# Kernel tuning notes

Measured on AMD Instinct MI355X. Metric: run time of the kernel, lower is better.

Reference implementation:

```python
import jax, jax.numpy as jnp
import numpy as np

EPS = 1e-15

def gmm_conv(x, row, col, pseudo, g_w, mu, sigma, root_w, bias):
    # x: [N,Fin], pseudo: [E,D], g_w: [Fin,K*Fout], mu/sigma: [K,D], root_w: [Fin,Fout]
    N = x.shape[0]
    K, D = mu.shape
    Fout = g_w.shape[1] // K
    gx = (x @ g_w).reshape(N, K, Fout)                       # per-node kernel transforms
    diff = pseudo[:, None, :] - mu[None, :, :]               # [E,K,D]
    gauss = jnp.exp(-0.5 * jnp.sum(diff * diff / (EPS + sigma[None] ** 2), axis=-1))  # [E,K]
    msg = jnp.einsum('ek,eko->eo', gauss, gx[row])           # [E,Fout]
    agg = jax.ops.segment_sum(msg, col, num_segments=N)      # scatter-add to targets
    cnt = jax.ops.segment_sum(jnp.ones((msg.shape[0],), x.dtype), col, num_segments=N)
    agg = agg / jnp.maximum(cnt, 1.0)[:, None]               # mean aggregation (GMMConv default)
    return agg + x @ root_w + bias

def setup_inputs() -> dict:
    key = jax.random.key(0)
    ks = jax.random.split(key, 12)
    N, E, F, H, C, K, D = 50000, 800000, 128, 64, 16, 8, 2
    return {
        'x': jax.random.normal(ks[0], (N, F), jnp.float32),
        'edge_index': jax.random.randint(ks[1], (2, E), 0, N, jnp.int64),
        'edge_attr': jax.random.uniform(ks[2], (E, D), jnp.float32),
        'g1_w': jax.random.normal(ks[3], (F, K * H), jnp.float32) * 0.1,
        'mu1': jax.random.normal(ks[4], (K, D), jnp.float32),
        'sigma1': jax.random.uniform(ks[5], (K, D), jnp.float32) + 0.5,
        'root1_w': jax.random.normal(ks[6], (F, H), jnp.float32) * 0.1,
        'bias1': jnp.zeros((H,), jnp.float32),
        'g2_w': jax.random.normal(ks[7], (H, K * C), jnp.float32) * 0.1,
        'mu2': jax.random.normal(ks[8], (K, D), jnp.float32),
        'sigma2': jax.random.uniform(ks[9], (K, D), jnp.float32) + 0.5,
        'root2_w': jax.random.normal(ks[10], (H, C), jnp.float32) * 0.1,
        'bias2': jnp.zeros((C,), jnp.float32),
    }

def reference(x, edge_index, edge_attr, g1_w, mu1, sigma1, root1_w, bias1,
              g2_w, mu2, sigma2, root2_w, bias2):
    row, col = edge_index[0], edge_index[1]
    # dropout p applied in eval mode -> identity
    h = jax.nn.elu(gmm_conv(x, row, col, edge_attr, g1_w, mu1, sigma1, root1_w, bias1))
    out = gmm_conv(h, row, col, edge_attr, g2_w, mu2, sigma2, root2_w, bias2)
    return jax.nn.log_softmax(out, axis=1)
```

## Files before the change

### kernel.cpp

```cpp
#include <hip/hip_runtime.h>
#include <hip/hip_bf16.h>
#include <hip/hip_fp16.h>
#include <math.h>


#define NF 128
#define NH 64
#define NC 16
#define Z1NODES 16
#define Z1CAP 448
#define E2NODES 16
#define E2CAP 320
#define GXST 160

typedef __bf16 v8bf __attribute__((ext_vector_type(8)));
typedef float v4f __attribute__((ext_vector_type(4)));

__device__ inline ushort f2bu(float x) {
  __hip_bfloat16 h = __float2bfloat16(x);
  return *(ushort*)&h;
}
__device__ inline uint packh2(float a, float b) {
  __half ha = __float2half_rn(a), hb = __float2half_rn(b);
  return (uint)(*(ushort*)&ha) | ((uint)(*(ushort*)&hb) << 16);
}
__device__ inline float2 unph2(uint u) {
  ushort a = (ushort)(u & 0xffff), b = (ushort)(u >> 16);
  return make_float2(__half2float(*(__half*)&a), __half2float(*(__half*)&b));
}
__device__ inline v8bf ld_frag(const ushort* p) {
  uint4 u = *(const uint4*)p;
  return __builtin_bit_cast(v8bf, u);
}

__global__ __launch_bounds__(256) void hist_kernel(const int* __restrict__ col,
                                                   int* __restrict__ counts, int E) {
  int e = blockIdx.x * 256 + threadIdx.x;
  if (e < E) atomicAdd(&counts[col[e]], 1);
}

__global__ __launch_bounds__(256) void scan1_kernel(const int* __restrict__ counts,
                                                    int* __restrict__ starts,
                                                    int* __restrict__ bsums) {
  __shared__ int wsum[4];
  const int t = threadIdx.x, lane = t & 63, wv = t >> 6;
  int4 v = ((const int4*)counts)[blockIdx.x * 256 + t];
  int tsum = v.x + v.y + v.z + v.w;
  int inc = tsum;
  #pragma unroll
  for (int off = 1; off < 64; off <<= 1) {
    int u = __shfl_up(inc, off, 64);
    if (lane >= off) inc += u;
  }
  if (lane == 63) wsum[wv] = inc;
  __syncthreads();
  int wpre = 0;
  for (int j = 0; j < wv; ++j) wpre += wsum[j];
  int excl = wpre + inc - tsum;
  int4 o;
  o.x = excl; o.y = o.x + v.x; o.z = o.y + v.y; o.w = o.z + v.z;
  ((int4*)starts)[blockIdx.x * 256 + t] = o;
  if (t == 255) bsums[blockIdx.x] = excl + tsum;
}

__global__ __launch_bounds__(64) void scan2_kernel(const int* __restrict__ bsums,
                                                   int* __restrict__ bofs, int NB) {
  int lane = threadIdx.x;
  int v = (lane < NB) ? bsums[lane] : 0;
  int inc = v;
  #pragma unroll
  for (int off = 1; off < 64; off <<= 1) {
    int u = __shfl_up(inc, off, 64);
    if (lane >= off) inc += u;
  }
  if (lane < NB) bofs[lane] = inc - v;
}

__global__ __launch_bounds__(256) void scan3_kernel(int* __restrict__ starts,
                                                    int* __restrict__ cursor,
                                                    const int* __restrict__ bofs) {
  int add = bofs[blockIdx.x];
  int idx = blockIdx.x * 256 + threadIdx.x;
  int4 s = ((int4*)starts)[idx];
  s.x += add; s.y += add; s.z += add; s.w += add;
  ((int4*)starts)[idx] = s;
  ((int4*)cursor)[idx] = s;
}

__global__ __launch_bounds__(256) void fill_kernel(
    const int* __restrict__ row, const int* __restrict__ col,
    const float* __restrict__ eattr,
    const float* __restrict__ mu1, const float* __restrict__ sg1,
    const float* __restrict__ mu2, const float* __restrict__ sg2,
    int* __restrict__ cursor, int* __restrict__ erow,
    uint4* __restrict__ ew1, uint4* __restrict__ ew2, int E) {
  int e = blockIdx.x * 256 + threadIdx.x;
  if (e >= E) return;
  int c = col[e];
  int pos = atomicAdd(&cursor[c], 1);
  float p0 = eattr[2 * e], p1 = eattr[2 * e + 1];
  float w1[8], w2[8];
  #pragma unroll
  for (int k = 0; k < 8; ++k) {
    float d0 = p0 - mu1[2 * k], d1 = p1 - mu1[2 * k + 1];
    float s0 = sg1[2 * k], s1 = sg1[2 * k + 1];
    w1[k] = __expf(-0.5f * (d0 * d0 / (1e-15f + s0 * s0) +
                            d1 * d1 / (1e-15f + s1 * s1)));
    float e0 = p0 - mu2[2 * k], e1 = p1 - mu2[2 * k + 1];
    float t0 = sg2[2 * k], t1 = sg2[2 * k + 1];
    w2[k] = __expf(-0.5f * (e0 * e0 / (1e-15f + t0 * t0) +
                            e1 * e1 / (1e-15f + t1 * t1)));
  }
  erow[pos] = row[e];
  ew1[pos] = make_uint4(packh2(w1[0], w1[1]), packh2(w1[2], w1[3]),
                        packh2(w1[4], w1[5]), packh2(w1[6], w1[7]));
  ew2[pos] = make_uint4(packh2(w2[0], w2[1]), packh2(w2[2], w2[3]),
                        packh2(w2[4], w2[5]), packh2(w2[6], w2[7]));
}

__global__ __launch_bounds__(256) void cast_x_kernel(const float* __restrict__ x,
                                                     ushort* __restrict__ A1, int N) {
  int idx = blockIdx.x * 256 + threadIdx.x;
  if (idx >= N * 32) return;
  int n = idx >> 5, c4 = idx & 31;
  float4 v = ((const float4*)x)[idx];
  ushort4 o;
  o.x = f2bu(v.x); o.y = f2bu(v.y); o.z = f2bu(v.z); o.w = f2bu(v.w);
  *(ushort4*)(A1 + (size_t)n * 1152 + 1024 + c4 * 4) = o;
}

__global__ __launch_bounds__(256) void prep_kernel(
    const float* __restrict__ g1w, const float* __restrict__ r1w,
    const float* __restrict__ g2w, const float* __restrict__ r2w,
    ushort* __restrict__ W1t, ushort* __restrict__ G2pT) {
  int i = blockIdx.x * 256 + threadIdx.x;
  if (i < 64 * 1152) {
    int h = i / 1152, j = i % 1152;
    float v = (j < 1024) ? g1w[(size_t)(j & 127) * 512 + (j >> 7) * 64 + h]
                         : r1w[(size_t)(j - 1024) * 64 + h];
    W1t[i] = f2bu(v);
  } else {
    int i2 = i - 64 * 1152;
    if (i2 < 144 * 64) {
      int cp = i2 / 64, f = i2 % 64;
      float v;
      if (cp < 128) {
        int kq = cp >> 5, rem = cp & 31;
        int o = rem >> 1, k = kq * 2 + (rem & 1);
        v = g2w[(size_t)f * 128 + k * 16 + o];
      } else {
        v = r2w[(size_t)f * 16 + (cp - 128)];
      }
      G2pT[i2] = f2bu(v);
    }
  }
}

__global__ __launch_bounds__(256) void z1_kernel(
    ushort* __restrict__ A1, const int* __restrict__ erow,
    const uint4* __restrict__ ew1, const int* __restrict__ starts, int N) {
  __shared__ __align__(16) float lw[Z1CAP + 8][8];
  __shared__ int loff[Z1CAP + 8];
  const int t = threadIdx.x, lane = t & 63, wv = t >> 6;
  const int base = (int)blockIdx.x * Z1NODES;
  const int S = starts[base];
  const int cl = min(starts[base + Z1NODES] - S, Z1CAP);
  for (int i = t; i < cl; i += 256) {
    loff[i] = erow[S + i] * 2304;
    uint4 qq = ew1[S + i];
    float2 a = unph2(qq.x), b = unph2(qq.y), c = unph2(qq.z), d = unph2(qq.w);
    *(float4*)&lw[i][0] = make_float4(a.x, a.y, b.x, b.y);
    *(float4*)&lw[i][4] = make_float4(c.x, c.y, d.x, d.y);
  }
  if (t < 8) {
    loff[cl + t] = 0;
    *(float4*)&lw[cl + t][0] = make_float4(0.f, 0.f, 0.f, 0.f);
    *(float4*)&lw[cl + t][4] = make_float4(0.f, 0.f, 0.f, 0.f);
  }
  __syncthreads();

  const char* xb = (const char*)(A1 + 1024) + (lane << 2);

  for (int i = 0; i < Z1NODES / 4; ++i) {
    const int n = base + wv * 4 + i;
    const int be = starts[n], ee = starts[n + 1];
    float a0[8], a1[8];
    #pragma unroll
    for (int k = 0; k < 8; ++k) { a0[k] = 0.f; a1[k] = 0.f; }

    const int reRel = min(ee - S, cl);
    for (int q = min(be - S, cl); q < reRel; q += 8) {
      int off[8];
      #pragma unroll
      for (int u = 0; u < 8; ++u) off[u] = loff[q + u];
      uint g[8];
      #pragma unroll
      for (int u = 0; u < 8; ++u) g[u] = *(const uint*)(xb + off[u]);
      #pragma unroll
      for (int u = 0; u < 8; ++u) {
        const bool ok = (q + u) < reRel;
        float4 wl = *(float4*)&lw[q + u][0];
        float4 wh = *(float4*)&lw[q + u][4];
        float f0 = ok ? __uint_as_float(g[u] << 16) : 0.f;
        float f1 = ok ? __uint_as_float(g[u] & 0xffff0000u) : 0.f;
        a0[0] = fmaf(wl.x, f0, a0[0]); a1[0] = fmaf(wl.x, f1, a1[0]);
        a0[1] = fmaf(wl.y, f0, a0[1]); a1[1] = fmaf(wl.y, f1, a1[1]);
        a0[2] = fmaf(wl.z, f0, a0[2]); a1[2] = fmaf(wl.z, f1, a1[2]);
        a0[3] = fmaf(wl.w, f0, a0[3]); a1[3] = fmaf(wl.w, f1, a1[3]);
        a0[4] = fmaf(wh.x, f0, a0[4]); a1[4] = fmaf(wh.x, f1, a1[4]);
        a0[5] = fmaf(wh.y, f0, a0[5]); a1[5] = fmaf(wh.y, f1, a1[5]);
        a0[6] = fmaf(wh.z, f0, a0[6]); a1[6] = fmaf(wh.z, f1, a1[6]);
        a0[7] = fmaf(wh.w, f0, a0[7]); a1[7] = fmaf(wh.w, f1, a1[7]);
      }
    }
    for (int j = max(S + reRel, be); j < ee; ++j) {
      uint4 qq = ew1[j];
      uint g = *(const uint*)(xb + erow[j] * 2304);
      float2 a = unph2(qq.x), b = unph2(qq.y), c = unph2(qq.z), d = unph2(qq.w);
      float f0 = __uint_as_float(g << 16);
      float f1 = __uint_as_float(g & 0xffff0000u);
      a0[0] = fmaf(a.x, f0, a0[0]); a1[0] = fmaf(a.x, f1, a1[0]);
      a0[1] = fmaf(a.y, f0, a0[1]); a1[1] = fmaf(a.y, f1, a1[1]);
      a0[2] = fmaf(b.x, f0, a0[2]); a1[2] = fmaf(b.x, f1, a1[2]);
      a0[3] = fmaf(b.y, f0, a0[3]); a1[3] = fmaf(b.y, f1, a1[3]);
      a0[4] = fmaf(c.x, f0, a0[4]); a1[4] = fmaf(c.x, f1, a1[4]);
      a0[5] = fmaf(c.y, f0, a0[5]); a1[5] = fmaf(c.y, f1, a1[5]);
      a0[6] = fmaf(d.x, f0, a0[6]); a1[6] = fmaf(d.x, f1, a1[6]);
      a0[7] = fmaf(d.y, f0, a0[7]); a1[7] = fmaf(d.y, f1, a1[7]);
    }
    const float inv = 1.f / fmaxf((float)(ee - be), 1.f);
    ushort* zr = A1 + (size_t)n * 1152;
    #pragma unroll
    for (int k = 0; k < 8; ++k) {
      uint pk = (uint)f2bu(a0[k] * inv) | ((uint)f2bu(a1[k] * inv) << 16);
      *(uint*)(zr + k * 128 + 2 * lane) = pk;
    }
  }
}

__global__ __launch_bounds__(256) void gemm1_mfma(
    const ushort* __restrict__ A1, const ushort* __restrict__ W1t,
    const float* __restrict__ b1, ushort* __restrict__ h_bf, int N) {
  __shared__ __align__(16) ushort As[2][64 * 32];
  __shared__ __align__(16) ushort Bs[2][64 * 32];
  const int t = threadIdx.x, lane = t & 63, wv = t >> 6;
  const int mfrag = lane & 15, quad = lane >> 4;
  const int m0 = (int)blockIdx.x * 64;
  const int st_r = t >> 2, st_c = (t & 3) * 8;
  const int st_o = st_r * 32 + st_c;
  const ushort* ag = A1 + (size_t)(m0 + st_r) * 1152 + st_c;
  const ushort* bg = W1t + (size_t)st_r * 1152 + st_c;

  {
    uint4 a0 = *(const uint4*)ag;
    uint4 b0 = *(const uint4*)bg;
    *(uint4*)(&As[0][st_o]) = a0;
    *(uint4*)(&Bs[0][st_o]) = b0;
  }
  __syncthreads();

  v4f acc[4];
  #pragma unroll
  for (int ct = 0; ct < 4; ++ct) acc[ct] = (v4f){0.f, 0.f, 0.f, 0.f};

  for (int kc = 0; kc < 36; ++kc) {
    const int cb = kc & 1, nb = cb ^ 1;
    uint4 an, bn;
    if (kc < 35) {
      an = *(const uint4*)(ag + (kc + 1) * 32);
      bn = *(const uint4*)(bg + (kc + 1) * 32);
    }
    v8bf a = ld_frag(&As[cb][(wv * 16 + mfrag) * 32 + quad * 8]);
    #pragma unroll
    for (int ct = 0; ct < 4; ++ct) {
      v8bf b = ld_frag(&Bs[cb][(ct * 16 + mfrag) * 32 + quad * 8]);
      acc[ct] = __builtin_amdgcn_mfma_f32_16x16x32_bf16(a, b, acc[ct], 0, 0, 0);
    }
    if (kc < 35) {
      *(uint4*)(&As[nb][st_o]) = an;
      *(uint4*)(&Bs[nb][st_o]) = bn;
      __syncthreads();
    }
  }
  #pragma unroll
  for (int ct = 0; ct < 4; ++ct) {
    const int colh = ct * 16 + mfrag;
    const float bc = b1[colh];
    #pragma unroll
    for (int r = 0; r < 4; ++r) {
      int node = m0 + wv * 16 + quad * 4 + r;
      if (node < N) {
        float v = acc[ct][r] + bc;
        v = v > 0.f ? v : expm1f(v);
        h_bf[(size_t)node * NH + colh] = f2bu(v);
      }
    }
  }
}

__global__ __launch_bounds__(256) void gemm2a_kernel(
    const ushort* __restrict__ h_bf, const ushort* __restrict__ G2pT,
    ushort* __restrict__ gx2e, int N) {
  const int t = threadIdx.x, lane = t & 63, wv = t >> 6;
  const int mfrag = lane & 15, quad = lane >> 4;
  const int m0 = (int)blockIdx.x * 64 + wv * 16;
  v4f acc[9];
  #pragma unroll
  for (int t9 = 0; t9 < 9; ++t9) acc[t9] = (v4f){0.f, 0.f, 0.f, 0.f};
  const ushort* arow = h_bf + (size_t)(m0 + mfrag) * 64 + quad * 8;
  const ushort* brow = G2pT + (size_t)mfrag * 64 + quad * 8;
  #pragma unroll
  for (int kc = 0; kc < 2; ++kc) {
    v8bf a = ld_frag(arow + kc * 32);
    #pragma unroll
    for (int t9 = 0; t9 < 9; ++t9) {
      v8bf b = ld_frag(brow + (size_t)t9 * 16 * 64 + kc * 32);
      acc[t9] = __builtin_amdgcn_mfma_f32_16x16x32_bf16(a, b, acc[t9], 0, 0, 0);
    }
  }
  #pragma unroll
  for (int t9 = 0; t9 < 9; ++t9) {
    #pragma unroll
    for (int r = 0; r < 4; ++r) {
      int node = m0 + quad * 4 + r;
      if (node < N)
        gx2e[(size_t)node * GXST + t9 * 16 + mfrag] = f2bu(acc[t9][r]);
    }
  }
}

__global__ __launch_bounds__(256) void edge2_kernel(
    const ushort* __restrict__ gx2e, const int* __restrict__ erow,
    const uint4* __restrict__ ew2, const int* __restrict__ starts,
    const float* __restrict__ b2, float* __restrict__ out, int N) {
  __shared__ __align__(16) float lw[E2CAP + 8][8];
  __shared__ int loff[E2CAP + 8];
  __shared__ float lb2[16];
  const int t = threadIdx.x, lane = t & 63, wv = t >> 6;
  const int base = (int)blockIdx.x * E2NODES;
  const int S = starts[base];
  const int cl = min(starts[base + E2NODES] - S, E2CAP);
  if (t < 16) lb2[t] = b2[t];
  for (int i = t; i < cl; i += 256) {
    loff[i] = erow[S + i] * 320;
    uint4 qq = ew2[S + i];
    float2 a = unph2(qq.x), b = unph2(qq.y), c = unph2(qq.z), d = unph2(qq.w);
    *(float4*)&lw[i][0] = make_float4(a.x, a.y, b.x, b.y);
    *(float4*)&lw[i][4] = make_float4(c.x, c.y, d.x, d.y);
  }
  if (t < 8) {
    loff[cl + t] = 0;
    *(float4*)&lw[cl + t][0] = make_float4(0.f, 0.f, 0.f, 0.f);
    *(float4*)&lw[cl + t][4] = make_float4(0.f, 0.f, 0.f, 0.f);
  }
  __syncthreads();

  const int o = lane & 15, kq = lane >> 4;
  const char* gb = (const char*)gx2e + kq * 64 + o * 4;

  for (int i = 0; i < E2NODES / 4; ++i) {
    const int n = base + wv * 4 + i;
    if (n >= N) continue;
    const int be = starts[n], ee = starts[n + 1];
    float acc0 = 0.f, acc1 = 0.f;
    const int reRel = min(ee - S, cl);
    for (int q = min(be - S, cl); q < reRel; q += 8) {
      int off[8];
      #pragma unroll
      for (int u = 0; u < 8; ++u) off[u] = loff[q + u];
      uint g[8];
      #pragma unroll
      for (int u = 0; u < 8; ++u) g[u] = *(const uint*)(gb + off[u]);
      #pragma unroll
      for (int u = 0; u < 8; ++u) {
        const bool ok = (q + u) < reRel;
        float2 w = *(float2*)&lw[q + u][kq * 2];
        float f0 = ok ? __uint_as_float(g[u] << 16) : 0.f;
        float f1 = ok ? __uint_as_float(g[u] & 0xffff0000u) : 0.f;
        acc0 = fmaf(w.x, f0, acc0);
        acc1 = fmaf(w.y, f1, acc1);
      }
    }
    for (int j = max(S + reRel, be); j < ee; ++j) {
      uint4 qq = ew2[j];
      uint comp = (kq == 0) ? qq.x : (kq == 1) ? qq.y : (kq == 2) ? qq.z : qq.w;
      float2 wp = unph2(comp);
      uint g = *(const uint*)(gb + erow[j] * 320);
      float f0 = __uint_as_float(g << 16);
      float f1 = __uint_as_float(g & 0xffff0000u);
      acc0 = fmaf(wp.x, f0, acc0);
      acc1 = fmaf(wp.y, f1, acc1);
    }
    float s = acc0 + acc1;
    s += __shfl_xor(s, 16, 64);
    s += __shfl_xor(s, 32, 64);
    const float inv = 1.f / fmaxf((float)(ee - be), 1.f);
    ushort ru = *((const ushort*)gx2e + (size_t)n * GXST + 128 + o);
    float root = __uint_as_float(((uint)ru) << 16);
    float v = s * inv + root + lb2[o];
    float mx = v;
    #pragma unroll
    for (int off = 8; off >= 1; off >>= 1) mx = fmaxf(mx, __shfl_xor(mx, off, 64));
    float sm = __expf(v - mx);
    #pragma unroll
    for (int off = 8; off >= 1; off >>= 1) sm += __shfl_xor(sm, off, 64);
    if (kq == 0) out[(size_t)n * NC + o] = v - mx - __logf(sm);
  }
}

extern "C" void kernel_launch(void* const* d_in, const int* in_sizes, int n_in,
                              void* d_out, int out_size, void* d_ws, size_t ws_size,
                              hipStream_t stream) {
  const float* x     = (const float*)d_in[0];
  const int*   eidx  = (const int*)d_in[1];
  const float* eattr = (const float*)d_in[2];
  const float* g1w   = (const float*)d_in[3];
  const float* mu1   = (const float*)d_in[4];
  const float* sg1   = (const float*)d_in[5];
  const float* r1w   = (const float*)d_in[6];
  const float* b1    = (const float*)d_in[7];
  const float* g2w   = (const float*)d_in[8];
  const float* mu2   = (const float*)d_in[9];
  const float* sg2   = (const float*)d_in[10];
  const float* r2w   = (const float*)d_in[11];
  const float* b2    = (const float*)d_in[12];

  const int N = in_sizes[0] / NF;
  const int E = in_sizes[1] / 2;
  const int* row = eidx;
  const int* col = eidx + E;
  const int N2 = (N + 63) & ~63;
  const int NP = (N + 1023) & ~1023;
  const int NB = NP / 1024;

  uint4* ew1   = (uint4*)d_ws;
  uint4* ew2   = ew1 + (size_t)E;
  ushort* A1   = (ushort*)(ew2 + (size_t)E);
  ushort* gx2e = A1;
  ushort* h_bf = A1 + (size_t)N2 * 1152;
  ushort* W1t  = h_bf + (size_t)N2 * NH;
  ushort* G2pT = W1t + (size_t)64 * 1152;
  int* erow    = (int*)(G2pT + (size_t)144 * 64);
  int* counts  = erow + (size_t)E;
  int* starts  = counts + NP;
  int* cursor  = starts + NP;
  int* bsums   = cursor + NP;
  int* bofs    = bsums + 64;

  hipMemsetAsync(counts, 0, (size_t)NP * sizeof(int), stream);
  hist_kernel<<<(E + 255) / 256, 256, 0, stream>>>(col, counts, E);
  scan1_kernel<<<NB, 256, 0, stream>>>(counts, starts, bsums);
  scan2_kernel<<<1, 64, 0, stream>>>(bsums, bofs, NB);
  scan3_kernel<<<NB, 256, 0, stream>>>(starts, cursor, bofs);
  fill_kernel<<<(E + 255) / 256, 256, 0, stream>>>(row, col, eattr, mu1, sg1,
                                                   mu2, sg2, cursor, erow,
                                                   ew1, ew2, E);
  cast_x_kernel<<<(N * 32 + 255) / 256, 256, 0, stream>>>(x, A1, N);
  prep_kernel<<<(64 * 1152 + 144 * 64 + 255) / 256, 256, 0, stream>>>(
      g1w, r1w, g2w, r2w, W1t, G2pT);

  z1_kernel<<<N / Z1NODES, 256, 0, stream>>>(A1, erow, ew1, starts, N);
  gemm1_mfma<<<N2 / 64, 256, 0, stream>>>(A1, W1t, b1, h_bf, N);
  gemm2a_kernel<<<N2 / 64, 256, 0, stream>>>(h_bf, G2pT, gx2e, N);
  edge2_kernel<<<(N + E2NODES - 1) / E2NODES, 256, 0, stream>>>(
      gx2e, erow, ew2, starts, b2, (float*)d_out, N);
}
```

Baseline: 329.5 us.

## Fuse setup kernels, single-pass scan, fuse both GEMMs, use packed FMA

Hist, x-cast and weight-prep now run as one setup kernel. The three-pass scan becomes a single pass with decoupled look-back, where each block spins on earlier blocks' aggregates. gemm1 and gemm2a are fused so the ELU output stays in shared memory instead of round-tripping through global memory. The z1 and edge2 accumulations use packed two-wide FMAs, and the workspace is reordered so gx2e aliases ew1. These cut launch count and memory traffic; the look-back spin relies on blocks being resident, and the aliasing relies on ew1 no longer being needed once z1 has run.

```diff
diff --git a/kernel.cpp b/kernel.cpp
--- a/kernel.cpp
+++ b/kernel.cpp
@@ -15,6 +15,7 @@
 
 typedef __bf16 v8bf __attribute__((ext_vector_type(8)));
 typedef float v4f __attribute__((ext_vector_type(4)));
+typedef float v2f __attribute__((ext_vector_type(2)));
 
 __device__ inline ushort f2bu(float x) {
   __hip_bfloat16 h = __float2bfloat16(x);
@@ -32,19 +33,65 @@
   uint4 u = *(const uint4*)p;
   return __builtin_bit_cast(v8bf, u);
 }
-
-__global__ __launch_bounds__(256) void hist_kernel(const int* __restrict__ col,
-                                                   int* __restrict__ counts, int E) {
-  int e = blockIdx.x * 256 + threadIdx.x;
-  if (e < E) atomicAdd(&counts[col[e]], 1);
-}
-
-__global__ __launch_bounds__(256) void scan1_kernel(const int* __restrict__ counts,
-                                                    int* __restrict__ starts,
-                                                    int* __restrict__ bsums) {
+__device__ inline v2f fma2(float w, v2f f, v2f a) {
+  return __builtin_elementwise_fma((v2f){w, w}, f, a);
+}
+
+__global__ __launch_bounds__(256) void setup_kernel(
+    const int* __restrict__ col, const float* __restrict__ x,
+    const float* __restrict__ g1w, const float* __restrict__ r1w,
+    const float* __restrict__ g2w, const float* __restrict__ r2w,
+    int* __restrict__ counts, ushort* __restrict__ A1,
+    ushort* __restrict__ W1t, ushort* __restrict__ G2pT,
+    int* __restrict__ bagg, int E, int N, int bh, int bc, int bp) {
+  const int b = blockIdx.x, t = threadIdx.x;
+  if (b < bh) {
+    int e = b * 256 + t;
+    if (e < E) atomicAdd(&counts[col[e]], 1);
+  } else if (b < bh + bc) {
+    int idx = (b - bh) * 256 + t;
+    if (idx < N * 32) {
+      int n = idx >> 5, c4 = idx & 31;
+      float4 v = ((const float4*)x)[idx];
+      ushort4 o;
+      o.x = f2bu(v.x); o.y = f2bu(v.y); o.z = f2bu(v.z); o.w = f2bu(v.w);
+      *(ushort4*)(A1 + (size_t)n * 1152 + 1024 + c4 * 4) = o;
+    }
+  } else if (b < bh + bc + bp) {
+    int i = (b - bh - bc) * 256 + t;
+    if (i < 64 * 1152) {
+      int h = i / 1152, j = i % 1152;
+      float v = (j < 1024) ? g1w[(size_t)(j & 127) * 512 + (j >> 7) * 64 + h]
+                           : r1w[(size_t)(j - 1024) * 64 + h];
+      W1t[i] = f2bu(v);
+    } else {
+      int i2 = i - 64 * 1152;
+      if (i2 < 144 * 64) {
+        int cp = i2 / 64, f = i2 % 64;
+        float v;
+        if (cp < 128) {
+          int kq = cp >> 5, rem = cp & 31;
+          int o = rem >> 1, k = kq * 2 + (rem & 1);
+          v = g2w[(size_t)f * 128 + k * 16 + o];
+        } else {
+          v = r2w[(size_t)f * 16 + (cp - 128)];
+        }
+        G2pT[i2] = f2bu(v);
+      }
+    }
+  } else {
+    if (t < 64) bagg[t] = 0;
+  }
+}
+
+__global__ __launch_bounds__(256) void scan_kernel(
+    const int* __restrict__ counts, int* __restrict__ starts,
+    int* __restrict__ cursor, int* __restrict__ bagg, int NB) {
   __shared__ int wsum[4];
+  __shared__ int s_pre;
   const int t = threadIdx.x, lane = t & 63, wv = t >> 6;
-  int4 v = ((const int4*)counts)[blockIdx.x * 256 + t];
+  const int b = blockIdx.x;
+  int4 v = ((const int4*)counts)[b * 256 + t];
   int tsum = v.x + v.y + v.z + v.w;
   int inc = tsum;
   #pragma unroll
@@ -54,37 +101,28 @@
   }
   if (lane == 63) wsum[wv] = inc;
   __syncthreads();
+  int agg = wsum[0] + wsum[1] + wsum[2] + wsum[3];
+  if (t == 0) atomicExch(&bagg[b], agg + 1);
+  __threadfence();
+  int pre = 0;
+  if (wv == 0) {
+    if (t < b) {
+      int val;
+      do { val = atomicAdd(&bagg[t], 0); } while (val == 0);
+      pre = val - 1;
+    }
+    #pragma unroll
+    for (int off = 32; off >= 1; off >>= 1) pre += __shfl_xor(pre, off, 64);
+    if (lane == 0) s_pre = pre;
+  }
+  __syncthreads();
   int wpre = 0;
   for (int j = 0; j < wv; ++j) wpre += wsum[j];
-  int excl = wpre + inc - tsum;
+  int excl = s_pre + wpre + inc - tsum;
   int4 o;
   o.x = excl; o.y = o.x + v.x; o.z = o.y + v.y; o.w = o.z + v.z;
-  ((int4*)starts)[blockIdx.x * 256 + t] = o;
-  if (t == 255) bsums[blockIdx.x] = excl + tsum;
-}
-
-__global__ __launch_bounds__(64) void scan2_kernel(const int* __restrict__ bsums,
-                                                   int* __restrict__ bofs, int NB) {
-  int lane = threadIdx.x;
-  int v = (lane < NB) ? bsums[lane] : 0;
-  int inc = v;
-  #pragma unroll
-  for (int off = 1; off < 64; off <<= 1) {
-    int u = __shfl_up(inc, off, 64);
-    if (lane >= off) inc += u;
-  }
-  if (lane < NB) bofs[lane] = inc - v;
-}
-
-__global__ __launch_bounds__(256) void scan3_kernel(int* __restrict__ starts,
-                                                    int* __restrict__ cursor,
-                                                    const int* __restrict__ bofs) {
-  int add = bofs[blockIdx.x];
-  int idx = blockIdx.x * 256 + threadIdx.x;
-  int4 s = ((int4*)starts)[idx];
-  s.x += add; s.y += add; s.z += add; s.w += add;
-  ((int4*)starts)[idx] = s;
-  ((int4*)cursor)[idx] = s;
+  ((int4*)starts)[b * 256 + t] = o;
+  ((int4*)cursor)[b * 256 + t] = o;
 }
 
 __global__ __launch_bounds__(256) void fill_kernel(
@@ -116,44 +154,6 @@
                         packh2(w1[4], w1[5]), packh2(w1[6], w1[7]));
   ew2[pos] = make_uint4(packh2(w2[0], w2[1]), packh2(w2[2], w2[3]),
                         packh2(w2[4], w2[5]), packh2(w2[6], w2[7]));
-}
-
-__global__ __launch_bounds__(256) void cast_x_kernel(const float* __restrict__ x,
-                                                     ushort* __restrict__ A1, int N) {
-  int idx = blockIdx.x * 256 + threadIdx.x;
-  if (idx >= N * 32) return;
-  int n = idx >> 5, c4 = idx & 31;
-  float4 v = ((const float4*)x)[idx];
-  ushort4 o;
-  o.x = f2bu(v.x); o.y = f2bu(v.y); o.z = f2bu(v.z); o.w = f2bu(v.w);
-  *(ushort4*)(A1 + (size_t)n * 1152 + 1024 + c4 * 4) = o;
-}
-
-__global__ __launch_bounds__(256) void prep_kernel(
-    const float* __restrict__ g1w, const float* __restrict__ r1w,
-    const float* __restrict__ g2w, const float* __restrict__ r2w,
-    ushort* __restrict__ W1t, ushort* __restrict__ G2pT) {
-  int i = blockIdx.x * 256 + threadIdx.x;
-  if (i < 64 * 1152) {
-    int h = i / 1152, j = i % 1152;
-    float v = (j < 1024) ? g1w[(size_t)(j & 127) * 512 + (j >> 7) * 64 + h]
-                         : r1w[(size_t)(j - 1024) * 64 + h];
-    W1t[i] = f2bu(v);
-  } else {
-    int i2 = i - 64 * 1152;
-    if (i2 < 144 * 64) {
-      int cp = i2 / 64, f = i2 % 64;
-      float v;
-      if (cp < 128) {
-        int kq = cp >> 5, rem = cp & 31;
-        int o = rem >> 1, k = kq * 2 + (rem & 1);
-        v = g2w[(size_t)f * 128 + k * 16 + o];
-      } else {
-        v = r2w[(size_t)f * 16 + (cp - 128)];
-      }
-      G2pT[i2] = f2bu(v);
-    }
-  }
 }
 
 __global__ __launch_bounds__(256) void z1_kernel(
@@ -184,9 +184,9 @@
   for (int i = 0; i < Z1NODES / 4; ++i) {
     const int n = base + wv * 4 + i;
     const int be = starts[n], ee = starts[n + 1];
-    float a0[8], a1[8];
-    #pragma unroll
-    for (int k = 0; k < 8; ++k) { a0[k] = 0.f; a1[k] = 0.f; }
+    v2f A[8];
+    #pragma unroll
+    for (int k = 0; k < 8; ++k) A[k] = (v2f){0.f, 0.f};
 
     const int reRel = min(ee - S, cl);
     for (int q = min(be - S, cl); q < reRel; q += 8) {
@@ -201,48 +201,48 @@
         const bool ok = (q + u) < reRel;
         float4 wl = *(float4*)&lw[q + u][0];
         float4 wh = *(float4*)&lw[q + u][4];
-        float f0 = ok ? __uint_as_float(g[u] << 16) : 0.f;
-        float f1 = ok ? __uint_as_float(g[u] & 0xffff0000u) : 0.f;
-        a0[0] = fmaf(wl.x, f0, a0[0]); a1[0] = fmaf(wl.x, f1, a1[0]);
-        a0[1] = fmaf(wl.y, f0, a0[1]); a1[1] = fmaf(wl.y, f1, a1[1]);
-        a0[2] = fmaf(wl.z, f0, a0[2]); a1[2] = fmaf(wl.z, f1, a1[2]);
-        a0[3] = fmaf(wl.w, f0, a0[3]); a1[3] = fmaf(wl.w, f1, a1[3]);
-        a0[4] = fmaf(wh.x, f0, a0[4]); a1[4] = fmaf(wh.x, f1, a1[4]);
-        a0[5] = fmaf(wh.y, f0, a0[5]); a1[5] = fmaf(wh.y, f1, a1[5]);
-        a0[6] = fmaf(wh.z, f0, a0[6]); a1[6] = fmaf(wh.z, f1, a1[6]);
-        a0[7] = fmaf(wh.w, f0, a0[7]); a1[7] = fmaf(wh.w, f1, a1[7]);
+        v2f F;
+        F.x = ok ? __uint_as_float(g[u] << 16) : 0.f;
+        F.y = ok ? __uint_as_float(g[u] & 0xffff0000u) : 0.f;
+        A[0] = fma2(wl.x, F, A[0]);
+        A[1] = fma2(wl.y, F, A[1]);
+        A[2] = fma2(wl.z, F, A[2]);
+        A[3] = fma2(wl.w, F, A[3]);
+        A[4] = fma2(wh.x, F, A[4]);
+        A[5] = fma2(wh.y, F, A[5]);
+        A[6] = fma2(wh.z, F, A[6]);
+        A[7] = fma2(wh.w, F, A[7]);
       }
     }
     for (int j = max(S + reRel, be); j < ee; ++j) {
       uint4 qq = ew1[j];
       uint g = *(const uint*)(xb + erow[j] * 2304);
       float2 a = unph2(qq.x), b = unph2(qq.y), c = unph2(qq.z), d = unph2(qq.w);
-      float f0 = __uint_as_float(g << 16);
-      float f1 = __uint_as_float(g & 0xffff0000u);
-      a0[0] = fmaf(a.x, f0, a0[0]); a1[0] = fmaf(a.x, f1, a1[0]);
-      a0[1] = fmaf(a.y, f0, a0[1]); a1[1] = fmaf(a.y, f1, a1[1]);
-      a0[2] = fmaf(b.x, f0, a0[2]); a1[2] = fmaf(b.x, f1, a1[2]);
-      a0[3] = fmaf(b.y, f0, a0[3]); a1[3] = fmaf(b.y, f1, a1[3]);
-      a0[4] = fmaf(c.x, f0, a0[4]); a1[4] = fmaf(c.x, f1, a1[4]);
-      a0[5] = fmaf(c.y, f0, a0[5]); a1[5] = fmaf(c.y, f1, a1[5]);
-      a0[6] = fmaf(d.x, f0, a0[6]); a1[6] = fmaf(d.x, f1, a1[6]);
-      a0[7] = fmaf(d.y, f0, a0[7]); a1[7] = fmaf(d.y, f1, a1[7]);
+      v2f F;
+      F.x = __uint_as_float(g << 16);
+      F.y = __uint_as_float(g & 0xffff0000u);
+      A[0] = fma2(a.x, F, A[0]); A[1] = fma2(a.y, F, A[1]);
+      A[2] = fma2(b.x, F, A[2]); A[3] = fma2(b.y, F, A[3]);
+      A[4] = fma2(c.x, F, A[4]); A[5] = fma2(c.y, F, A[5]);
+      A[6] = fma2(d.x, F, A[6]); A[7] = fma2(d.y, F, A[7]);
     }
     const float inv = 1.f / fmaxf((float)(ee - be), 1.f);
     ushort* zr = A1 + (size_t)n * 1152;
     #pragma unroll
     for (int k = 0; k < 8; ++k) {
-      uint pk = (uint)f2bu(a0[k] * inv) | ((uint)f2bu(a1[k] * inv) << 16);
+      uint pk = (uint)f2bu(A[k].x * inv) | ((uint)f2bu(A[k].y * inv) << 16);
       *(uint*)(zr + k * 128 + 2 * lane) = pk;
     }
   }
 }
 
-__global__ __launch_bounds__(256) void gemm1_mfma(
+__global__ __launch_bounds__(256) void gemm12_kernel(
     const ushort* __restrict__ A1, const ushort* __restrict__ W1t,
-    const float* __restrict__ b1, ushort* __restrict__ h_bf, int N) {
+    const float* __restrict__ b1, const ushort* __restrict__ G2pT,
+    ushort* __restrict__ gx2e, int N) {
   __shared__ __align__(16) ushort As[2][64 * 32];
   __shared__ __align__(16) ushort Bs[2][64 * 32];
+  __shared__ __align__(16) ushort Hs[64][72];
   const int t = threadIdx.x, lane = t & 63, wv = t >> 6;
   const int mfrag = lane & 15, quad = lane >> 4;
   const int m0 = (int)blockIdx.x * 64;
@@ -288,43 +288,33 @@
     const float bc = b1[colh];
     #pragma unroll
     for (int r = 0; r < 4; ++r) {
-      int node = m0 + wv * 16 + quad * 4 + r;
-      if (node < N) {
-        float v = acc[ct][r] + bc;
-        v = v > 0.f ? v : expm1f(v);
-        h_bf[(size_t)node * NH + colh] = f2bu(v);
-      }
-    }
-  }
-}
-
-__global__ __launch_bounds__(256) void gemm2a_kernel(
-    const ushort* __restrict__ h_bf, const ushort* __restrict__ G2pT,
-    ushort* __restrict__ gx2e, int N) {
-  const int t = threadIdx.x, lane = t & 63, wv = t >> 6;
-  const int mfrag = lane & 15, quad = lane >> 4;
-  const int m0 = (int)blockIdx.x * 64 + wv * 16;
-  v4f acc[9];
-  #pragma unroll
-  for (int t9 = 0; t9 < 9; ++t9) acc[t9] = (v4f){0.f, 0.f, 0.f, 0.f};
-  const ushort* arow = h_bf + (size_t)(m0 + mfrag) * 64 + quad * 8;
+      float v = acc[ct][r] + bc;
+      v = v > 0.f ? v : expm1f(v);
+      Hs[wv * 16 + quad * 4 + r][colh] = f2bu(v);
+    }
+  }
+  __syncthreads();
+
+  v4f acc2[9];
+  #pragma unroll
+  for (int t9 = 0; t9 < 9; ++t9) acc2[t9] = (v4f){0.f, 0.f, 0.f, 0.f};
   const ushort* brow = G2pT + (size_t)mfrag * 64 + quad * 8;
   #pragma unroll
   for (int kc = 0; kc < 2; ++kc) {
-    v8bf a = ld_frag(arow + kc * 32);
+    v8bf a = ld_frag(&Hs[wv * 16 + mfrag][quad * 8 + kc * 32]);
     #pragma unroll
     for (int t9 = 0; t9 < 9; ++t9) {
       v8bf b = ld_frag(brow + (size_t)t9 * 16 * 64 + kc * 32);
-      acc[t9] = __builtin_amdgcn_mfma_f32_16x16x32_bf16(a, b, acc[t9], 0, 0, 0);
+      acc2[t9] = __builtin_amdgcn_mfma_f32_16x16x32_bf16(a, b, acc2[t9], 0, 0, 0);
     }
   }
   #pragma unroll
   for (int t9 = 0; t9 < 9; ++t9) {
     #pragma unroll
     for (int r = 0; r < 4; ++r) {
-      int node = m0 + quad * 4 + r;
+      int node = m0 + wv * 16 + quad * 4 + r;
       if (node < N)
-        gx2e[(size_t)node * GXST + t9 * 16 + mfrag] = f2bu(acc[t9][r]);
+        gx2e[(size_t)node * GXST + t9 * 16 + mfrag] = f2bu(acc2[t9][r]);
     }
   }
 }
@@ -362,7 +352,7 @@
     const int n = base + wv * 4 + i;
     if (n >= N) continue;
     const int be = starts[n], ee = starts[n + 1];
-    float acc0 = 0.f, acc1 = 0.f;
+    v2f ACC = (v2f){0.f, 0.f};
     const int reRel = min(ee - S, cl);
     for (int q = min(be - S, cl); q < reRel; q += 8) {
       int off[8];
@@ -374,11 +364,11 @@
       #pragma unroll
       for (int u = 0; u < 8; ++u) {
         const bool ok = (q + u) < reRel;
-        float2 w = *(float2*)&lw[q + u][kq * 2];
-        float f0 = ok ? __uint_as_float(g[u] << 16) : 0.f;
-        float f1 = ok ? __uint_as_float(g[u] & 0xffff0000u) : 0.f;
-        acc0 = fmaf(w.x, f0, acc0);
-        acc1 = fmaf(w.y, f1, acc1);
+        v2f W = *(v2f*)&lw[q + u][kq * 2];
+        v2f F;
+        F.x = ok ? __uint_as_float(g[u] << 16) : 0.f;
+        F.y = ok ? __uint_as_float(g[u] & 0xffff0000u) : 0.f;
+        ACC = __builtin_elementwise_fma(W, F, ACC);
       }
     }
     for (int j = max(S + reRel, be); j < ee; ++j) {
@@ -386,12 +376,10 @@
       uint comp = (kq == 0) ? qq.x : (kq == 1) ? qq.y : (kq == 2) ? qq.z : qq.w;
       float2 wp = unph2(comp);
       uint g = *(const uint*)(gb + erow[j] * 320);
-      float f0 = __uint_as_float(g << 16);
-      float f1 = __uint_as_float(g & 0xffff0000u);
-      acc0 = fmaf(wp.x, f0, acc0);
-      acc1 = fmaf(wp.y, f1, acc1);
-    }
-    float s = acc0 + acc1;
+      ACC.x = fmaf(wp.x, __uint_as_float(g << 16), ACC.x);
+      ACC.y = fmaf(wp.y, __uint_as_float(g & 0xffff0000u), ACC.y);
+    }
+    float s = ACC.x + ACC.y;
     s += __shfl_xor(s, 16, 64);
     s += __shfl_xor(s, 32, 64);
     const float inv = 1.f / fmaxf((float)(ee - be), 1.f);
@@ -433,35 +421,33 @@
   const int NP = (N + 1023) & ~1023;
   const int NB = NP / 1024;
 
-  uint4* ew1   = (uint4*)d_ws;
-  uint4* ew2   = ew1 + (size_t)E;
-  ushort* A1   = (ushort*)(ew2 + (size_t)E);
-  ushort* gx2e = A1;
-  ushort* h_bf = A1 + (size_t)N2 * 1152;
-  ushort* W1t  = h_bf + (size_t)N2 * NH;
+  char* wsb = (char*)d_ws;
+  uint4* ew2   = (uint4*)wsb;
+  uint4* ew1   = (uint4*)(wsb + (size_t)E * 16);
+  ushort* gx2e = (ushort*)ew1;
+  size_t ew1span = (size_t)N2 * 320;
+  if (ew1span < (size_t)E * 16) ew1span = (size_t)E * 16;
+  ushort* A1   = (ushort*)(wsb + (size_t)E * 16 + ew1span);
+  ushort* W1t  = A1 + (size_t)N2 * 1152;
   ushort* G2pT = W1t + (size_t)64 * 1152;
   int* erow    = (int*)(G2pT + (size_t)144 * 64);
   int* counts  = erow + (size_t)E;
   int* starts  = counts + NP;
   int* cursor  = starts + NP;
-  int* bsums   = cursor + NP;
-  int* bofs    = bsums + 64;
+  int* bagg    = cursor + NP;
+
+  const int bh = (E + 255) / 256;
+  const int bc = (N * 32 + 255) / 256;
+  const int bp = (64 * 1152 + 144 * 64 + 255) / 256;
 
   hipMemsetAsync(counts, 0, (size_t)NP * sizeof(int), stream);
-  hist_kernel<<<(E + 255) / 256, 256, 0, stream>>>(col, counts, E);
-  scan1_kernel<<<NB, 256, 0, stream>>>(counts, starts, bsums);
-  scan2_kernel<<<1, 64, 0, stream>>>(bsums, bofs, NB);
-  scan3_kernel<<<NB, 256, 0, stream>>>(starts, cursor, bofs);
-  fill_kernel<<<(E + 255) / 256, 256, 0, stream>>>(row, col, eattr, mu1, sg1,
-                                                   mu2, sg2, cursor, erow,
-                                                   ew1, ew2, E);
-  cast_x_kernel<<<(N * 32 + 255) / 256, 256, 0, stream>>>(x, A1, N);
-  prep_kernel<<<(64 * 1152 + 144 * 64 + 255) / 256, 256, 0, stream>>>(
-      g1w, r1w, g2w, r2w, W1t, G2pT);
-
+  setup_kernel<<<bh + bc + bp + 1, 256, 0, stream>>>(
+      col, x, g1w, r1w, g2w, r2w, counts, A1, W1t, G2pT, bagg, E, N, bh, bc, bp);
+  scan_kernel<<<NB, 256, 0, stream>>>(counts, starts, cursor, bagg, NB);
+  fill_kernel<<<bh, 256, 0, stream>>>(row, col, eattr, mu1, sg1, mu2, sg2,
+                                      cursor, erow, ew1, ew2, E);
   z1_kernel<<<N / Z1NODES, 256, 0, stream>>>(A1, erow, ew1, starts, N);
-  gemm1_mfma<<<N2 / 64, 256, 0, stream>>>(A1, W1t, b1, h_bf, N);
-  gemm2a_kernel<<<N2 / 64, 256, 0, stream>>>(h_bf, G2pT, gx2e, N);
+  gemm12_kernel<<<N2 / 64, 256, 0, stream>>>(A1, W1t, b1, G2pT, gx2e, N);
   edge2_kernel<<<(N + E2NODES - 1) / E2NODES, 256, 0, stream>>>(
       gx2e, erow, ew2, starts, b2, (float*)d_out, N);
 }
```

Result: no change. 334.6 us (+1.5%).
